# Kernel tuning notes

Hardware: AMD Instinct MI355X
Metric: run time of the kernel (lower is better)

Reference implementation:

```python
import jax, jax.numpy as jnp
import numpy as np

DIM = 96
D_STATE = 16
EXPAND = 2
D_INNER = EXPAND * DIM
DT_RANK = (DIM + 15) // 16  # 6
B, H, W = 2, 64, 64
K = 4  # scan directions


def _ln(x, w, b, eps=1e-5):
    mu = x.mean(-1, keepdims=True)
    var = x.var(-1, keepdims=True)
    return (x - mu) / jnp.sqrt(var + eps) * w + b


def setup_inputs() -> dict:
    key = jax.random.key(0)
    ks = jax.random.split(key, 10)
    f = jnp.float32
    x = jax.random.normal(ks[0], (B, H, W, DIM), dtype=f)
    y = jax.random.normal(ks[1], (B, H, W, DIM), dtype=f)
    inp = {
        'x': x,
        'y': y,
        'ln_w': jnp.ones((DIM,), f),
        'ln_b': jnp.zeros((DIM,), f),
        'in_proj_w': jax.random.normal(ks[2], (2 * D_INNER, DIM), f) * 0.05,
        'conv_w': jax.random.normal(ks[3], (D_INNER, 1, 3, 3), f) * 0.1,
        'conv_b': jnp.zeros((D_INNER,), f),
        'x_proj_w': jax.random.normal(ks[4], (K, DT_RANK + 2 * D_STATE, D_INNER), f) * 0.05,
        'dt_w': jax.random.normal(ks[5], (K, D_INNER, DT_RANK), f) * 0.1,
        'dt_b': jax.random.normal(ks[6], (K, D_INNER), f) * 0.1,
        'A_log': jnp.broadcast_to(jnp.log(jnp.arange(1, D_STATE + 1, dtype=f)), (K, D_INNER, D_STATE)),
        'Ds': jnp.ones((K, D_INNER), f),
        'out_norm_w': jnp.ones((D_INNER,), f),
        'out_norm_b': jnp.zeros((D_INNER,), f),
        'out_proj_w': jax.random.normal(ks[7], (DIM, D_INNER), f) * 0.05,
    }
    return inp


def _fwd(x, y, ln_w, ln_b, in_proj_w, conv_w, conv_b, x_proj_w, dt_w, dt_b,
         A_log, Ds, out_norm_w, out_norm_b, out_proj_w):
    Bsz, Hh, Ww, C = x.shape
    Din = conv_w.shape[0]
    N = A_log.shape[-1]
    R = dt_w.shape[-1]
    L = Hh * Ww

    diff = jnp.abs(x - y)                       # TemporalSpectrumBlock abs-diff
    h = _ln(diff, ln_w, ln_b)                   # VSSBlock ln_1
    xz = h @ in_proj_w.T                        # (B,H,W,2*Din)
    xm, z = jnp.split(xz, 2, axis=-1)
    xm = xm.transpose(0, 3, 1, 2)               # (B,Din,H,W)
    xm = jax.lax.conv_general_dilated(
        xm, conv_w, (1, 1), 'SAME', feature_group_count=Din,
        dimension_numbers=('NCHW', 'OIHW', 'NCHW')) + conv_b[None, :, None, None]
    xm = jax.nn.silu(xm)

    # 4-directional sequences (B,4,Din,L)
    x0 = xm.reshape(Bsz, Din, L)
    x1 = xm.transpose(0, 1, 3, 2).reshape(Bsz, Din, L)
    xs = jnp.stack([x0, x1], axis=1)
    xs = jnp.concatenate([xs, jnp.flip(xs, axis=-1)], axis=1)

    x_dbl = jnp.einsum('bkdl,kcd->bkcl', xs, x_proj_w)
    dts, Bs, Cs = jnp.split(x_dbl, [R, R + N], axis=2)   # (B,4,R,L),(B,4,N,L),(B,4,N,L)
    dts = jnp.einsum('bkrl,kdr->bkdl', dts, dt_w)
    delta = jax.nn.softplus(dts + dt_b[None, :, :, None])  # (B,4,Din,L)

    A = -jnp.exp(A_log)                                    # (4,Din,N)
    dA = jnp.exp(delta[..., None] * A[None, :, :, None, :])          # (B,4,Din,L,N)
    dBu = delta[..., None] * Bs.transpose(0, 1, 3, 2)[:, :, None] * xs[..., None]

    dA_t = dA.transpose(3, 0, 1, 2, 4)    # (L,B,4,Din,N)
    dBu_t = dBu.transpose(3, 0, 1, 2, 4)
    C_t = Cs.transpose(3, 0, 1, 2)        # (L,B,4,N)
    h0 = jnp.zeros((Bsz, 4, Din, N), dtype=x.dtype)

    def step(hc, inp):
        a, bu, c = inp
        hc = a * hc + bu
        yv = jnp.einsum('bkdn,bkn->bkd', hc, c)
        return hc, yv

    _, ys = jax.lax.scan(step, h0, (dA_t, dBu_t, C_t))    # (L,B,4,Din)
    ys = ys.transpose(1, 2, 3, 0)                          # (B,4,Din,L)
    out_y = ys + Ds[None, :, :, None] * xs

    inv_y = jnp.flip(out_y[:, 2:4], axis=-1)
    wh_y = out_y[:, 1].reshape(Bsz, Din, Ww, Hh).transpose(0, 1, 3, 2).reshape(Bsz, Din, L)
    invwh_y = inv_y[:, 1].reshape(Bsz, Din, Ww, Hh).transpose(0, 1, 3, 2).reshape(Bsz, Din, L)
    yc = out_y[:, 0] + inv_y[:, 0] + wh_y + invwh_y        # (B,Din,L)
    yc = yc.transpose(0, 2, 1).reshape(Bsz, Hh, Ww, Din)

    yn = _ln(yc, out_norm_w, out_norm_b)
    out = (yn * jax.nn.silu(z)) @ out_proj_w.T
    return diff + out                                      # residual around the block


def reference(x, y, ln_w, ln_b, in_proj_w, conv_w, conv_b, x_proj_w, dt_w, dt_b,
              A_log, Ds, out_norm_w, out_norm_b, out_proj_w):
    return _fwd(x, y, ln_w, ln_b, in_proj_w, conv_w, conv_b, x_proj_w, dt_w, dt_b,
                A_log, Ds, out_norm_w, out_norm_b, out_proj_w)
```

## Files before the change

### kernel.cpp

```cpp
#include <hip/hip_runtime.h>
#include <math.h>

#define DIMC 96
#define DIN  192
#define NST  16
#define RNK  6
#define KD   4
#define HH   64
#define WWD  64
#define LL   4096
#define BB   2
#define NC   256
#define CH   16
#define CPK  48

__device__ __forceinline__ int pos_of(int k, int l) {
    int t = ((l & 63) << 6) | (l >> 6);
    switch (k) {
        case 0: return l;
        case 1: return t;
        case 2: return LL - 1 - l;
        default: return ((((LL-1-l) & 63) << 6) | ((LL-1-l) >> 6));
    }
}

__device__ __forceinline__ float silu_f(float v) {
    return v / (1.f + __expf(-v));
}

__global__ __launch_bounds__(256) void k0_prep(
    const float* __restrict__ Win, const float* __restrict__ Wout,
    const float* __restrict__ xpw,
    float* __restrict__ WinT, float* __restrict__ WoutT, float* __restrict__ wT3)
{
    int idx = blockIdx.x*256 + threadIdx.x;
    int stride = gridDim.x*256;
    for (int i = idx; i < 96*384; i += stride) {
        int j = i / 384, o = i - j*384;
        WinT[i] = Win[o*96 + j];
    }
    for (int i = idx; i < 192*96; i += stride) {
        int j = i / 96, o = i - j*96;
        WoutT[i] = Wout[o*192 + j];
    }
    for (int i = idx; i < KD*192*CPK; i += stride) {
        int kk = i / (192*CPK); int rem = i - kk*192*CPK;
        int j = rem / CPK, c = rem - j*CPK;
        float v = 0.f;
        if (c < 16)       v = xpw[((size_t)kk*(RNK+2*NST) + RNK + c)*DIN + j];
        else if (c < 32)  v = xpw[((size_t)kk*(RNK+2*NST) + RNK + NST + (c-16))*DIN + j];
        else if (c < 38)  v = xpw[((size_t)kk*(RNK+2*NST) + (c-32))*DIN + j];
        wT3[i] = v;
    }
}

__global__ __launch_bounds__(1024) void k1_ln_inproj(
    const float* __restrict__ x, const float* __restrict__ y,
    const float* __restrict__ lnw, const float* __restrict__ lnb,
    const float* __restrict__ WinT,
    float* __restrict__ diff, float* __restrict__ xm, float* __restrict__ zbuf)
{
    __shared__ float hT[96*65];
    __shared__ float ps1[16*64], ps2[16*64];
    __shared__ float mus[64], rss[64];
    int t = threadIdx.x;
    int ptile = blockIdx.x >> 1, cgrp = blockIdx.x & 1;
    int p0 = ptile*64;

    #pragma unroll
    for (int s = 0; s < 6; s++) {
        int i = t + 1024*s;
        float v = fabsf(x[(size_t)p0*96 + i] - y[(size_t)p0*96 + i]);
        if (cgrp == 0) diff[(size_t)p0*96 + i] = v;
        int pos = i / 96, ch = i - pos*96;
        hT[ch*65 + pos] = v;
    }
    __syncthreads();
    {
        int pos = t & 63, part = t >> 6;
        float s1 = 0.f, s2 = 0.f;
        #pragma unroll
        for (int m = 0; m < 6; m++) {
            float v = hT[(part*6 + m)*65 + pos];
            s1 += v; s2 += v*v;
        }
        ps1[part*64 + pos] = s1; ps2[part*64 + pos] = s2;
    }
    __syncthreads();
    if (t < 64) {
        float S1 = 0.f, S2 = 0.f;
        #pragma unroll
        for (int i = 0; i < 16; i++) { S1 += ps1[i*64 + t]; S2 += ps2[i*64 + t]; }
        float mu = S1 * (1.f/96.f);
        float var = S2 * (1.f/96.f) - mu*mu;
        mus[t] = mu; rss[t] = rsqrtf(var + 1e-5f);
    }
    __syncthreads();
    #pragma unroll
    for (int s = 0; s < 6; s++) {
        int i = t + 1024*s;
        int pos = i / 96, ch = i - pos*96;
        hT[ch*65 + pos] = (hT[ch*65 + pos] - mus[pos]) * rss[pos] * lnw[ch] + lnb[ch];
    }
    __syncthreads();

    int w = __builtin_amdgcn_readfirstlane(t >> 6);
    int lane = t & 63;
    int c0 = cgrp*192 + w*12;
    const float* wp = WinT + c0;
    float acc[12];
    #pragma unroll
    for (int cc = 0; cc < 12; cc++) acc[cc] = 0.f;
    #pragma unroll 2
    for (int j = 0; j < 96; j++) {
        float u = hT[j*65 + lane];
        const float* wrow = wp + j*384;
        #pragma unroll
        for (int cc = 0; cc < 12; cc++) acc[cc] += u * wrow[cc];
    }
    size_t p = (size_t)(p0 + lane);
    float* dst = (c0 < 192) ? (xm + p*192 + c0) : (zbuf + p*192 + (c0 - 192));
    #pragma unroll
    for (int q = 0; q < 3; q++)
        *(float4*)&dst[4*q] = make_float4(acc[4*q], acc[4*q+1], acc[4*q+2], acc[4*q+3]);
}

__global__ __launch_bounds__(192) void k2_conv(
    const float* __restrict__ xm, const float* __restrict__ cw,
    const float* __restrict__ cb, float* __restrict__ xconv,
    float* __restrict__ xconvT)
{
    int p = blockIdx.x;
    int d = threadIdx.x;
    int b = p >> 12;
    int l = p & (LL - 1);
    int hh = l >> 6, ww = l & 63;
    float acc = cb[d];
    const float* wd = cw + d*9;
    #pragma unroll
    for (int di = -1; di <= 1; di++) {
        int h2 = hh + di;
        if ((unsigned)h2 < HH) {
            #pragma unroll
            for (int dj = -1; dj <= 1; dj++) {
                int w2 = ww + dj;
                if ((unsigned)w2 < WWD)
                    acc += wd[(di+1)*3 + (dj+1)] * xm[((size_t)b*LL + h2*WWD + w2)*DIN + d];
            }
        }
    }
    float v = silu_f(acc);
    xconv[(size_t)p*DIN + d] = v;
    int tl = ((l & 63) << 6) | (l >> 6);
    xconvT[((size_t)b*LL + tl)*DIN + d] = v;
}

__global__ __launch_bounds__(512) void k3_xproj(
    const float* __restrict__ xconv, const float* __restrict__ wT3,
    float* __restrict__ XDK)
{
    __shared__ float uT[192*65];
    int t = threadIdx.x;
    int ptile = blockIdx.x >> 1, wgrp = blockIdx.x & 1;
    int p0 = ptile*64;

    #pragma unroll
    for (int s = 0; s < 24; s++) {
        int i = t + 512*s;
        int pos = i / 192, ch = i - pos*192;
        uT[ch*65 + pos] = xconv[(size_t)(p0 + pos)*192 + ch];
    }
    __syncthreads();

    int w = __builtin_amdgcn_readfirstlane(t >> 6);
    int slot = wgrp*8 + w;
    int k = slot >> 2, cq = slot & 3;
    int lane = t & 63;
    int c0 = cq*12;
    const float* wp = wT3 + (size_t)k*192*CPK + c0;
    float acc[12];
    #pragma unroll
    for (int cc = 0; cc < 12; cc++) acc[cc] = 0.f;
    #pragma unroll 2
    for (int j = 0; j < 192; j++) {
        float u = uT[j*65 + lane];
        const float* wrow = wp + j*CPK;
        #pragma unroll
        for (int cc = 0; cc < 12; cc++) acc[cc] += u * wrow[cc];
    }
    int p = p0 + lane;
    int b = p >> 12;
    int s = p & (LL - 1);
    int ts = ((s & 63) << 6) | (s >> 6);
    int l;
    switch (k) {
        case 0: l = s; break;
        case 1: l = ts; break;
        case 2: l = LL - 1 - s; break;
        default: l = LL - 1 - ts; break;
    }
    float* dst = XDK + ((size_t)(b*KD + k)*LL + l)*CPK + c0;
    #pragma unroll
    for (int q = 0; q < 3; q++)
        *(float4*)&dst[4*q] = make_float4(acc[4*q], acc[4*q+1], acc[4*q+2], acc[4*q+3]);
}

__global__ __launch_bounds__(192) void k4_scanA(
    const float* __restrict__ xconv, const float* __restrict__ xconvT,
    const float* __restrict__ XDK,
    const float* __restrict__ dtw, const float* __restrict__ dtb,
    const float* __restrict__ A_log,
    float* __restrict__ Sarr, float* __restrict__ Q)
{
    int blk = blockIdx.x;
    int c  = blk & (NC - 1);
    int bk = blk >> 8;
    int k  = bk & 3;
    int b  = bk >> 2;
    int d  = threadIdx.x;
    const float* xc = (k & 1) ? xconvT : xconv;
    float dw[RNK];
    #pragma unroll
    for (int r = 0; r < RNK; r++) dw[r] = dtw[((size_t)k*DIN + d)*RNK + r];
    float bias = dtb[k*DIN + d];
    float A[NST];
    #pragma unroll
    for (int n = 0; n < NST; n++) A[n] = -__expf(A_log[((size_t)k*DIN + d)*NST + n]);
    bool fastA = true;
    #pragma unroll
    for (int n = 1; n < NST; n++)
        fastA = fastA && (fabsf(A[n] - (float)(n+1)*A[0]) <= 1e-4f*(float)(n+1));

    float h[NST];
    #pragma unroll
    for (int n = 0; n < NST; n++) h[n] = 0.f;
    float S = 0.f;

    size_t rb = ((size_t)bk*LL + c*CH);
    if (fastA) {
        #pragma unroll 4
        for (int step = 0; step < CH; step++) {
            const float* rec = XDK + (rb + step)*CPK;
            float dl = bias;
            #pragma unroll
            for (int r = 0; r < RNK; r++) dl += rec[32 + r] * dw[r];
            dl = (dl > 20.f) ? dl : __logf(1.f + __expf(dl));
            int l = c*CH + step;
            int li = (k < 2) ? l : (LL - 1 - l);
            float uu = xc[((size_t)b*LL + li)*DIN + d];
            float du = dl * uu;
            S += dl;
            float e1 = __expf(dl * A[0]);
            float e2 = e1*e1, e4 = e2*e2;
            float p0 = e1, p1 = e2, p2 = e2*e1, p3 = e4;
            #pragma unroll
            for (int g = 0; g < 4; g++) {
                h[4*g+0] = p0*h[4*g+0] + du*rec[4*g+0];
                h[4*g+1] = p1*h[4*g+1] + du*rec[4*g+1];
                h[4*g+2] = p2*h[4*g+2] + du*rec[4*g+2];
                h[4*g+3] = p3*h[4*g+3] + du*rec[4*g+3];
                if (g < 3) { p0 *= e4; p1 *= e4; p2 *= e4; p3 *= e4; }
            }
        }
    } else {
        #pragma unroll 2
        for (int step = 0; step < CH; step++) {
            const float* rec = XDK + (rb + step)*CPK;
            float dl = bias;
            #pragma unroll
            for (int r = 0; r < RNK; r++) dl += rec[32 + r] * dw[r];
            dl = (dl > 20.f) ? dl : __logf(1.f + __expf(dl));
            int l = c*CH + step;
            int li = (k < 2) ? l : (LL - 1 - l);
            float uu = xc[((size_t)b*LL + li)*DIN + d];
            float du = dl * uu;
            S += dl;
            #pragma unroll
            for (int n = 0; n < NST; n++) {
                float a = __expf(dl * A[n]);
                h[n] = a*h[n] + du*rec[n];
            }
        }
    }
    Sarr[(size_t)blk*DIN + d] = S;
    size_t qb = (size_t)blk*NST*DIN + d;
    #pragma unroll
    for (int n = 0; n < NST; n++) Q[qb + n*DIN] = h[n];
}

__global__ __launch_bounds__(256) void k5_scanB(
    const float* __restrict__ A_log, const float* __restrict__ Sarr,
    float* __restrict__ Q)
{
    int idx = blockIdx.x*256 + threadIdx.x;
    if (idx >= BB*KD*NST*DIN) return;
    int d = idx % DIN;
    int rest = idx / DIN;
    int n = rest % NST; rest /= NST;
    int k = rest & 3;
    int b = rest >> 2;
    int bk = b*KD + k;
    float A = -__expf(A_log[((size_t)k*DIN + d)*NST + n]);
    size_t qstride = (size_t)NST*DIN;
    size_t qbase = (size_t)bk*NC*qstride + n*DIN + d;
    size_t sbase = (size_t)bk*NC*DIN + d;
    float h = 0.f;
    #pragma unroll 4
    for (int c = 0; c < NC; c++) {
        float s = Sarr[sbase + c*DIN];
        float q = Q[qbase + c*qstride];
        Q[qbase + c*qstride] = h;
        h = __expf(A*s)*h + q;
    }
}

__global__ __launch_bounds__(192) void k6_scanC(
    const float* __restrict__ xconv, const float* __restrict__ xconvT,
    const float* __restrict__ XDK,
    const float* __restrict__ dtw, const float* __restrict__ dtb,
    const float* __restrict__ A_log, const float* __restrict__ Ds,
    const float* __restrict__ Q, float* __restrict__ outy)
{
    int blk = blockIdx.x;
    int c  = blk & (NC - 1);
    int bk = blk >> 8;
    int k  = bk & 3;
    int b  = bk >> 2;
    int d  = threadIdx.x;
    const float* xc = (k & 1) ? xconvT : xconv;
    float dw[RNK];
    #pragma unroll
    for (int r = 0; r < RNK; r++) dw[r] = dtw[((size_t)k*DIN + d)*RNK + r];
    float bias = dtb[k*DIN + d];
    float A[NST];
    #pragma unroll
    for (int n = 0; n < NST; n++) A[n] = -__expf(A_log[((size_t)k*DIN + d)*NST + n]);
    bool fastA = true;
    #pragma unroll
    for (int n = 1; n < NST; n++)
        fastA = fastA && (fabsf(A[n] - (float)(n+1)*A[0]) <= 1e-4f*(float)(n+1));
    float h[NST];
    size_t qb = (size_t)blk*NST*DIN + d;
    #pragma unroll
    for (int n = 0; n < NST; n++) h[n] = Q[qb + n*DIN];
    float Dv = Ds[k*DIN + d];

    size_t rb = ((size_t)bk*LL + c*CH);
    if (fastA) {
        #pragma unroll 4
        for (int step = 0; step < CH; step++) {
            const float* rec = XDK + (rb + step)*CPK;
            float dl = bias;
            #pragma unroll
            for (int r = 0; r < RNK; r++) dl += rec[32 + r] * dw[r];
            dl = (dl > 20.f) ? dl : __logf(1.f + __expf(dl));
            int l = c*CH + step;
            int li = (k < 2) ? l : (LL - 1 - l);
            float uu = xc[((size_t)b*LL + li)*DIN + d];
            int sp = pos_of(k, l);
            float du = dl * uu;
            float e1 = __expf(dl * A[0]);
            float e2 = e1*e1, e4 = e2*e2;
            float p0 = e1, p1 = e2, p2 = e2*e1, p3 = e4;
            float yv = 0.f;
            #pragma unroll
            for (int g = 0; g < 4; g++) {
                h[4*g+0] = p0*h[4*g+0] + du*rec[4*g+0];
                h[4*g+1] = p1*h[4*g+1] + du*rec[4*g+1];
                h[4*g+2] = p2*h[4*g+2] + du*rec[4*g+2];
                h[4*g+3] = p3*h[4*g+3] + du*rec[4*g+3];
                yv += h[4*g+0]*rec[16+4*g+0] + h[4*g+1]*rec[16+4*g+1]
                    + h[4*g+2]*rec[16+4*g+2] + h[4*g+3]*rec[16+4*g+3];
                if (g < 3) { p0 *= e4; p1 *= e4; p2 *= e4; p3 *= e4; }
            }
            outy[((size_t)bk*LL + sp)*DIN + d] = yv + Dv*uu;
        }
    } else {
        #pragma unroll 2
        for (int step = 0; step < CH; step++) {
            const float* rec = XDK + (rb + step)*CPK;
            float dl = bias;
            #pragma unroll
            for (int r = 0; r < RNK; r++) dl += rec[32 + r] * dw[r];
            dl = (dl > 20.f) ? dl : __logf(1.f + __expf(dl));
            int l = c*CH + step;
            int li = (k < 2) ? l : (LL - 1 - l);
            float uu = xc[((size_t)b*LL + li)*DIN + d];
            int sp = pos_of(k, l);
            float du = dl * uu;
            float yv = 0.f;
            #pragma unroll
            for (int n = 0; n < NST; n++) {
                float a = __expf(dl * A[n]);
                h[n] = a*h[n] + du*rec[n];
                yv += h[n] * rec[16 + n];
            }
            outy[((size_t)bk*LL + sp)*DIN + d] = yv + Dv*uu;
        }
    }
}

__global__ __launch_bounds__(192) void k7a_comb(
    const float* __restrict__ outy, const float* __restrict__ zbuf,
    const float* __restrict__ onw, const float* __restrict__ onb,
    float* __restrict__ gbuf)
{
    __shared__ float red1[3], red2[3];
    __shared__ float s_mu, s_rs;
    int p = blockIdx.x;
    int d = threadIdx.x;
    int b = p >> 12;
    const size_t seg = (size_t)LL*DIN;
    size_t base = ((size_t)(b*KD)*LL + (p & (LL-1)))*DIN + d;

    float yc = outy[base] + outy[base + seg] + outy[base + 2*seg] + outy[base + 3*seg];

    float s1 = yc, s2 = yc*yc;
    #pragma unroll
    for (int off = 32; off > 0; off >>= 1) {
        s1 += __shfl_down(s1, off);
        s2 += __shfl_down(s2, off);
    }
    int wid = d >> 6, lane = d & 63;
    if (lane == 0) { red1[wid] = s1; red2[wid] = s2; }
    __syncthreads();
    if (d == 0) {
        float S1 = red1[0] + red1[1] + red1[2];
        float S2 = red2[0] + red2[1] + red2[2];
        float mu = S1 * (1.f/192.f);
        float var = S2 * (1.f/192.f) - mu*mu;
        s_mu = mu; s_rs = rsqrtf(var + 1e-5f);
    }
    __syncthreads();
    float yn = (yc - s_mu) * s_rs * onw[d] + onb[d];
    gbuf[(size_t)p*DIN + d] = yn * silu_f(zbuf[(size_t)p*DIN + d]);
}

__global__ __launch_bounds__(256) void k7b_gemm(
    const float* __restrict__ gbuf, const float* __restrict__ diff,
    const float* __restrict__ WoutT, float* __restrict__ out)
{
    __shared__ float gT[192*65];
    int t = threadIdx.x;
    int ptile = blockIdx.x >> 2, cq = blockIdx.x & 3;
    int p0 = ptile*64;

    #pragma unroll
    for (int s = 0; s < 48; s++) {
        int i = t + 256*s;
        int pos = i / 192, ch = i - pos*192;
        gT[ch*65 + pos] = gbuf[(size_t)(p0 + pos)*192 + ch];
    }
    __syncthreads();

    int w = __builtin_amdgcn_readfirstlane(t >> 6);
    int lane = t & 63;
    int c0 = cq*24 + w*6;
    const float* wp = WoutT + c0;
    float acc[6];
    #pragma unroll
    for (int cc = 0; cc < 6; cc++) acc[cc] = 0.f;
    #pragma unroll 2
    for (int j = 0; j < 192; j++) {
        float u = gT[j*65 + lane];
        const float* wrow = wp + j*96;
        #pragma unroll
        for (int cc = 0; cc < 6; cc++) acc[cc] += u * wrow[cc];
    }
    size_t p = (size_t)(p0 + lane);
    #pragma unroll
    for (int q = 0; q < 3; q++) {
        float2 dv = *(const float2*)&diff[p*96 + c0 + 2*q];
        *(float2*)&out[p*96 + c0 + 2*q] = make_float2(acc[2*q] + dv.x, acc[2*q+1] + dv.y);
    }
}

extern "C" void kernel_launch(void* const* d_in, const int* in_sizes, int n_in,
                              void* d_out, int out_size, void* d_ws, size_t ws_size,
                              hipStream_t stream)
{
    const float* x       = (const float*)d_in[0];
    const float* y       = (const float*)d_in[1];
    const float* ln_w    = (const float*)d_in[2];
    const float* ln_b    = (const float*)d_in[3];
    const float* in_proj = (const float*)d_in[4];
    const float* conv_w  = (const float*)d_in[5];
    const float* conv_b  = (const float*)d_in[6];
    const float* x_proj  = (const float*)d_in[7];
    const float* dt_w    = (const float*)d_in[8];
    const float* dt_b    = (const float*)d_in[9];
    const float* A_log   = (const float*)d_in[10];
    const float* Ds      = (const float*)d_in[11];
    const float* onw     = (const float*)d_in[12];
    const float* onb     = (const float*)d_in[13];
    const float* out_w   = (const float*)d_in[14];
    float* out = (float*)d_out;

    float* ws     = (float*)d_ws;
    float* diff   = ws;
    float* zbuf   = diff   + 786432;
    float* xm     = zbuf   + 1572864;
    float* xconv  = xm     + 1572864;
    float* xconvT = xconv  + 1572864;
    float* XDK    = xconvT + 1572864;
    float* outy   = XDK    + 1572864;
    float* Qbuf   = outy   + 6291456;
    float* Sarr   = Qbuf   + 6291456;
    float* gbuf   = Sarr   + 393216;
    float* WinT   = gbuf   + 1572864;
    float* WoutT  = WinT   + 36864;
    float* wT3    = WoutT  + 18432;

    const int BL = BB * LL;

    hipLaunchKernelGGL(k0_prep, dim3(144), dim3(256), 0, stream,
                       in_proj, out_w, x_proj, WinT, WoutT, wT3);
    hipLaunchKernelGGL(k1_ln_inproj, dim3(BL/64*2), dim3(1024), 0, stream,
                       x, y, ln_w, ln_b, WinT, diff, xm, zbuf);
    hipLaunchKernelGGL(k2_conv, dim3(BL), dim3(DIN), 0, stream,
                       xm, conv_w, conv_b, xconv, xconvT);
    hipLaunchKernelGGL(k3_xproj, dim3(BL/64*2), dim3(512), 0, stream,
                       xconv, wT3, XDK);
    hipLaunchKernelGGL(k4_scanA, dim3(BB*KD*NC), dim3(DIN), 0, stream,
                       xconv, xconvT, XDK, dt_w, dt_b, A_log, Sarr, Qbuf);
    hipLaunchKernelGGL(k5_scanB, dim3((BB*KD*NST*DIN + 255)/256), dim3(256), 0, stream,
                       A_log, Sarr, Qbuf);
    hipLaunchKernelGGL(k6_scanC, dim3(BB*KD*NC), dim3(DIN), 0, stream,
                       xconv, xconvT, XDK, dt_w, dt_b, A_log, Ds, Qbuf, outy);
    hipLaunchKernelGGL(k7a_comb, dim3(BL), dim3(DIN), 0, stream,
                       outy, zbuf, onw, onb, gbuf);
    hipLaunchKernelGGL(k7b_gemm, dim3(128*4), dim3(256), 0, stream,
                       gbuf, diff, WoutT, out);
}
```

Measured before the change: 276.4 us.

## Fuse three-pass chunked scan into single-pass decoupled look-back scan

Replaces the three scan kernels (per-chunk aggregate, serial carry propagation, chunk rescan) with one kernel. Blocks take a dynamic ticket, compute the local scan with zero initial state, publish their aggregate and look back through predecessors' flags to get an inclusive prefix state. Outputs are then corrected with exp(A*cumsum)·hin·C instead of recomputing the whole chunk. This removes the second pass over XDK/xconv and two launches. In exchange it adds spin-wait synchronization, per-thread register arrays for yv and cs, and a serial look-back latency chain across 256 chunks.

```diff
diff --git a/kernel.cpp b/kernel.cpp
--- a/kernel.cpp
+++ b/kernel.cpp
@@ -13,6 +13,7 @@
 #define NC   256
 #define CH   16
 #define CPK  48
+#define NBLK (BB*KD*NC)
 
 __device__ __forceinline__ int pos_of(int k, int l) {
     int t = ((l & 63) << 6) | (l >> 6);
@@ -26,6 +27,13 @@
 
 __device__ __forceinline__ float silu_f(float v) {
     return v / (1.f + __expf(-v));
+}
+
+__global__ __launch_bounds__(256) void kz_zero(int* __restrict__ flags, int* __restrict__ ticket)
+{
+    int i = blockIdx.x*256 + threadIdx.x;
+    if (i < NBLK) flags[i] = 0;
+    if (i == 0) *ticket = 0;
 }
 
 __global__ __launch_bounds__(256) void k0_prep(
@@ -205,20 +213,27 @@
         *(float4*)&dst[4*q] = make_float4(acc[4*q], acc[4*q+1], acc[4*q+2], acc[4*q+3]);
 }
 
-__global__ __launch_bounds__(192) void k4_scanA(
+__global__ __launch_bounds__(192) void k4_single(
     const float* __restrict__ xconv, const float* __restrict__ xconvT,
     const float* __restrict__ XDK,
     const float* __restrict__ dtw, const float* __restrict__ dtb,
-    const float* __restrict__ A_log,
-    float* __restrict__ Sarr, float* __restrict__ Q)
-{
-    int blk = blockIdx.x;
-    int c  = blk & (NC - 1);
-    int bk = blk >> 8;
+    const float* __restrict__ A_log, const float* __restrict__ Ds,
+    float* __restrict__ Sagg, float* __restrict__ Qagg, float* __restrict__ Hinc,
+    int* __restrict__ flags, int* __restrict__ ticket,
+    float* __restrict__ outy)
+{
+    __shared__ int s_tick;
+    __shared__ int s_flag;
+    int d = threadIdx.x;
+    if (d == 0) s_tick = atomicAdd(ticket, 1);
+    __syncthreads();
+    int t  = s_tick;
+    int c  = t & (NC - 1);
+    int bk = t >> 8;
     int k  = bk & 3;
     int b  = bk >> 2;
-    int d  = threadIdx.x;
     const float* xc = (k & 1) ? xconvT : xconv;
+
     float dw[RNK];
     #pragma unroll
     for (int r = 0; r < RNK; r++) dw[r] = dtw[((size_t)k*DIN + d)*RNK + r];
@@ -226,19 +241,22 @@
     float A[NST];
     #pragma unroll
     for (int n = 0; n < NST; n++) A[n] = -__expf(A_log[((size_t)k*DIN + d)*NST + n]);
+    float A0 = A[0];
     bool fastA = true;
     #pragma unroll
     for (int n = 1; n < NST; n++)
-        fastA = fastA && (fabsf(A[n] - (float)(n+1)*A[0]) <= 1e-4f*(float)(n+1));
+        fastA = fastA && (fabsf(A[n] - (float)(n+1)*A0) <= 1e-4f*(float)(n+1));
+    float Dv = Ds[k*DIN + d];
 
     float h[NST];
     #pragma unroll
     for (int n = 0; n < NST; n++) h[n] = 0.f;
+    float yv[CH], cs[CH];
     float S = 0.f;
-
     size_t rb = ((size_t)bk*LL + c*CH);
+
     if (fastA) {
-        #pragma unroll 4
+        #pragma unroll
         for (int step = 0; step < CH; step++) {
             const float* rec = XDK + (rb + step)*CPK;
             float dl = bias;
@@ -249,21 +267,25 @@
             int li = (k < 2) ? l : (LL - 1 - l);
             float uu = xc[((size_t)b*LL + li)*DIN + d];
             float du = dl * uu;
-            S += dl;
-            float e1 = __expf(dl * A[0]);
+            S += dl; cs[step] = S;
+            float e1 = __expf(dl * A0);
             float e2 = e1*e1, e4 = e2*e2;
             float p0 = e1, p1 = e2, p2 = e2*e1, p3 = e4;
+            float yvv = Dv*uu;
             #pragma unroll
             for (int g = 0; g < 4; g++) {
                 h[4*g+0] = p0*h[4*g+0] + du*rec[4*g+0];
                 h[4*g+1] = p1*h[4*g+1] + du*rec[4*g+1];
                 h[4*g+2] = p2*h[4*g+2] + du*rec[4*g+2];
                 h[4*g+3] = p3*h[4*g+3] + du*rec[4*g+3];
+                yvv += h[4*g+0]*rec[16+4*g+0] + h[4*g+1]*rec[16+4*g+1]
+                     + h[4*g+2]*rec[16+4*g+2] + h[4*g+3]*rec[16+4*g+3];
                 if (g < 3) { p0 *= e4; p1 *= e4; p2 *= e4; p3 *= e4; }
             }
+            yv[step] = yvv;
         }
     } else {
-        #pragma unroll 2
+        #pragma unroll
         for (int step = 0; step < CH; step++) {
             const float* rec = XDK + (rb + step)*CPK;
             float dl = bias;
@@ -274,128 +296,104 @@
             int li = (k < 2) ? l : (LL - 1 - l);
             float uu = xc[((size_t)b*LL + li)*DIN + d];
             float du = dl * uu;
-            S += dl;
+            S += dl; cs[step] = S;
+            float yvv = Dv*uu;
             #pragma unroll
             for (int n = 0; n < NST; n++) {
                 float a = __expf(dl * A[n]);
                 h[n] = a*h[n] + du*rec[n];
+                yvv += h[n] * rec[16 + n];
             }
-        }
-    }
-    Sarr[(size_t)blk*DIN + d] = S;
-    size_t qb = (size_t)blk*NST*DIN + d;
-    #pragma unroll
-    for (int n = 0; n < NST; n++) Q[qb + n*DIN] = h[n];
-}
-
-__global__ __launch_bounds__(256) void k5_scanB(
-    const float* __restrict__ A_log, const float* __restrict__ Sarr,
-    float* __restrict__ Q)
-{
-    int idx = blockIdx.x*256 + threadIdx.x;
-    if (idx >= BB*KD*NST*DIN) return;
-    int d = idx % DIN;
-    int rest = idx / DIN;
-    int n = rest % NST; rest /= NST;
-    int k = rest & 3;
-    int b = rest >> 2;
-    int bk = b*KD + k;
-    float A = -__expf(A_log[((size_t)k*DIN + d)*NST + n]);
-    size_t qstride = (size_t)NST*DIN;
-    size_t qbase = (size_t)bk*NC*qstride + n*DIN + d;
-    size_t sbase = (size_t)bk*NC*DIN + d;
-    float h = 0.f;
-    #pragma unroll 4
-    for (int c = 0; c < NC; c++) {
-        float s = Sarr[sbase + c*DIN];
-        float q = Q[qbase + c*qstride];
-        Q[qbase + c*qstride] = h;
-        h = __expf(A*s)*h + q;
-    }
-}
-
-__global__ __launch_bounds__(192) void k6_scanC(
-    const float* __restrict__ xconv, const float* __restrict__ xconvT,
-    const float* __restrict__ XDK,
-    const float* __restrict__ dtw, const float* __restrict__ dtb,
-    const float* __restrict__ A_log, const float* __restrict__ Ds,
-    const float* __restrict__ Q, float* __restrict__ outy)
-{
-    int blk = blockIdx.x;
-    int c  = blk & (NC - 1);
-    int bk = blk >> 8;
-    int k  = bk & 3;
-    int b  = bk >> 2;
-    int d  = threadIdx.x;
-    const float* xc = (k & 1) ? xconvT : xconv;
-    float dw[RNK];
-    #pragma unroll
-    for (int r = 0; r < RNK; r++) dw[r] = dtw[((size_t)k*DIN + d)*RNK + r];
-    float bias = dtb[k*DIN + d];
-    float A[NST];
-    #pragma unroll
-    for (int n = 0; n < NST; n++) A[n] = -__expf(A_log[((size_t)k*DIN + d)*NST + n]);
-    bool fastA = true;
-    #pragma unroll
-    for (int n = 1; n < NST; n++)
-        fastA = fastA && (fabsf(A[n] - (float)(n+1)*A[0]) <= 1e-4f*(float)(n+1));
-    float h[NST];
-    size_t qb = (size_t)blk*NST*DIN + d;
-    #pragma unroll
-    for (int n = 0; n < NST; n++) h[n] = Q[qb + n*DIN];
-    float Dv = Ds[k*DIN + d];
-
-    size_t rb = ((size_t)bk*LL + c*CH);
+            yv[step] = yvv;
+        }
+    }
+
+    size_t sb = (size_t)t*DIN + d;
+    size_t qb = (size_t)t*NST*DIN + d;
+    if (c > 0) {
+        Sagg[sb] = S;
+        #pragma unroll
+        for (int n = 0; n < NST; n++) Qagg[qb + n*DIN] = h[n];
+        __threadfence();
+        __syncthreads();
+        if (d == 0) __hip_atomic_store(flags + t, 1, __ATOMIC_RELEASE, __HIP_MEMORY_SCOPE_AGENT);
+    }
+
+    float hin[NST];
+    #pragma unroll
+    for (int n = 0; n < NST; n++) hin[n] = 0.f;
+    if (c > 0) {
+        float Mn[NST];
+        #pragma unroll
+        for (int n = 0; n < NST; n++) Mn[n] = 1.f;
+        int j = t - 1;
+        while (true) {
+            if (d == 0) {
+                int f;
+                do {
+                    f = __hip_atomic_load(flags + j, __ATOMIC_ACQUIRE, __HIP_MEMORY_SCOPE_AGENT);
+                    if (!f) __builtin_amdgcn_s_sleep(2);
+                } while (!f);
+                s_flag = f;
+            }
+            __syncthreads();
+            int f = s_flag;
+            __syncthreads();
+            if (f == 2) {
+                #pragma unroll
+                for (int n = 0; n < NST; n++)
+                    hin[n] += Mn[n] * Hinc[(size_t)j*NST*DIN + n*DIN + d];
+                break;
+            } else {
+                float Sj = Sagg[(size_t)j*DIN + d];
+                #pragma unroll
+                for (int n = 0; n < NST; n++) {
+                    hin[n] += Mn[n] * Qagg[(size_t)j*NST*DIN + n*DIN + d];
+                    Mn[n] *= __expf(A[n] * Sj);
+                }
+                j--;
+            }
+        }
+    }
+
+    {
+        #pragma unroll
+        for (int n = 0; n < NST; n++)
+            Hinc[qb + n*DIN] = h[n] + __expf(A[n]*S) * hin[n];
+        __threadfence();
+        __syncthreads();
+        if (d == 0) __hip_atomic_store(flags + t, 2, __ATOMIC_RELEASE, __HIP_MEMORY_SCOPE_AGENT);
+    }
+
     if (fastA) {
-        #pragma unroll 4
+        #pragma unroll
         for (int step = 0; step < CH; step++) {
             const float* rec = XDK + (rb + step)*CPK;
-            float dl = bias;
-            #pragma unroll
-            for (int r = 0; r < RNK; r++) dl += rec[32 + r] * dw[r];
-            dl = (dl > 20.f) ? dl : __logf(1.f + __expf(dl));
+            float E = __expf(A0 * cs[step]);
+            float E2 = E*E, E4 = E2*E2;
+            float p0 = E, p1 = E2, p2 = E2*E, p3 = E4;
+            float corr = 0.f;
+            #pragma unroll
+            for (int g = 0; g < 4; g++) {
+                corr += p0*hin[4*g+0]*rec[16+4*g+0] + p1*hin[4*g+1]*rec[16+4*g+1]
+                      + p2*hin[4*g+2]*rec[16+4*g+2] + p3*hin[4*g+3]*rec[16+4*g+3];
+                if (g < 3) { p0 *= E4; p1 *= E4; p2 *= E4; p3 *= E4; }
+            }
             int l = c*CH + step;
-            int li = (k < 2) ? l : (LL - 1 - l);
-            float uu = xc[((size_t)b*LL + li)*DIN + d];
             int sp = pos_of(k, l);
-            float du = dl * uu;
-            float e1 = __expf(dl * A[0]);
-            float e2 = e1*e1, e4 = e2*e2;
-            float p0 = e1, p1 = e2, p2 = e2*e1, p3 = e4;
-            float yv = 0.f;
-            #pragma unroll
-            for (int g = 0; g < 4; g++) {
-                h[4*g+0] = p0*h[4*g+0] + du*rec[4*g+0];
-                h[4*g+1] = p1*h[4*g+1] + du*rec[4*g+1];
-                h[4*g+2] = p2*h[4*g+2] + du*rec[4*g+2];
-                h[4*g+3] = p3*h[4*g+3] + du*rec[4*g+3];
-                yv += h[4*g+0]*rec[16+4*g+0] + h[4*g+1]*rec[16+4*g+1]
-                    + h[4*g+2]*rec[16+4*g+2] + h[4*g+3]*rec[16+4*g+3];
-                if (g < 3) { p0 *= e4; p1 *= e4; p2 *= e4; p3 *= e4; }
-            }
-            outy[((size_t)bk*LL + sp)*DIN + d] = yv + Dv*uu;
+            outy[((size_t)bk*LL + sp)*DIN + d] = yv[step] + corr;
         }
     } else {
-        #pragma unroll 2
+        #pragma unroll
         for (int step = 0; step < CH; step++) {
             const float* rec = XDK + (rb + step)*CPK;
-            float dl = bias;
-            #pragma unroll
-            for (int r = 0; r < RNK; r++) dl += rec[32 + r] * dw[r];
-            dl = (dl > 20.f) ? dl : __logf(1.f + __expf(dl));
+            float corr = 0.f;
+            #pragma unroll
+            for (int n = 0; n < NST; n++)
+                corr += __expf(A[n]*cs[step]) * hin[n] * rec[16 + n];
             int l = c*CH + step;
-            int li = (k < 2) ? l : (LL - 1 - l);
-            float uu = xc[((size_t)b*LL + li)*DIN + d];
             int sp = pos_of(k, l);
-            float du = dl * uu;
-            float yv = 0.f;
-            #pragma unroll
-            for (int n = 0; n < NST; n++) {
-                float a = __expf(dl * A[n]);
-                h[n] = a*h[n] + du*rec[n];
-                yv += h[n] * rec[16 + n];
-            }
-            outy[((size_t)bk*LL + sp)*DIN + d] = yv + Dv*uu;
+            outy[((size_t)bk*LL + sp)*DIN + d] = yv[step] + corr;
         }
     }
 }
@@ -504,15 +502,20 @@
     float* xconvT = xconv  + 1572864;
     float* XDK    = xconvT + 1572864;
     float* outy   = XDK    + 1572864;
-    float* Qbuf   = outy   + 6291456;
-    float* Sarr   = Qbuf   + 6291456;
-    float* gbuf   = Sarr   + 393216;
+    float* Qagg   = outy   + 6291456;
+    float* Hinc   = Qagg   + 6291456;
+    float* Sagg   = Hinc   + 6291456;
+    float* gbuf   = Sagg   + 393216;
     float* WinT   = gbuf   + 1572864;
     float* WoutT  = WinT   + 36864;
     float* wT3    = WoutT  + 18432;
+    int*   flags  = (int*)(wT3 + 36864);
+    int*   ticket = flags + NBLK;
 
     const int BL = BB * LL;
 
+    hipLaunchKernelGGL(kz_zero, dim3((NBLK + 255)/256), dim3(256), 0, stream,
+                       flags, ticket);
     hipLaunchKernelGGL(k0_prep, dim3(144), dim3(256), 0, stream,
                        in_proj, out_w, x_proj, WinT, WoutT, wT3);
     hipLaunchKernelGGL(k1_ln_inproj, dim3(BL/64*2), dim3(1024), 0, stream,
@@ -521,12 +524,9 @@
                        xm, conv_w, conv_b, xconv, xconvT);
     hipLaunchKernelGGL(k3_xproj, dim3(BL/64*2), dim3(512), 0, stream,
                        xconv, wT3, XDK);
-    hipLaunchKernelGGL(k4_scanA, dim3(BB*KD*NC), dim3(DIN), 0, stream,
-                       xconv, xconvT, XDK, dt_w, dt_b, A_log, Sarr, Qbuf);
-    hipLaunchKernelGGL(k5_scanB, dim3((BB*KD*NST*DIN + 255)/256), dim3(256), 0, stream,
-                       A_log, Sarr, Qbuf);
-    hipLaunchKernelGGL(k6_scanC, dim3(BB*KD*NC), dim3(DIN), 0, stream,
-                       xconv, xconvT, XDK, dt_w, dt_b, A_log, Ds, Qbuf, outy);
+    hipLaunchKernelGGL(k4_single, dim3(NBLK), dim3(DIN), 0, stream,
+                       xconv, xconvT, XDK, dt_w, dt_b, A_log, Ds,
+                       Sagg, Qagg, Hinc, flags, ticket, outy);
     hipLaunchKernelGGL(k7a_comb, dim3(BL), dim3(DIN), 0, stream,
                        outy, zbuf, onw, onb, gbuf);
     hipLaunchKernelGGL(k7b_gemm, dim3(128*4), dim3(256), 0, stream,
```

Measured after the change: 1.079 ms. 3.9x slower.
